# Kernel tuning notes

Measured on AMD Instinct MI355X. Metric: run time of the kernel, lower is better.

The kernel has to match this reference:

```python
import jax, jax.numpy as jnp
import numpy as np

B = 2048; E = 6; H = 4; D = 128; DH = D // H
LTXT = 24; CS = 20; JD = 7; SD = 16; LD = 32; K = 2
NLB = 4; NLD = 3; VOCAB = 512; DFF = 4 * D


def _ln(x, s, b, eps=1e-5):
    m = x.mean(-1, keepdims=True)
    v = ((x - m) ** 2).mean(-1, keepdims=True)
    return (x - m) * jax.lax.rsqrt(v + eps) * s + b


def _mha(xq, xkv, Wqkv, bqkv, Wo, bo, key_pad=None):
    # torch nn.MultiheadAttention, batch_first, eval (no dropout)
    Wq, Wk, Wv = jnp.split(Wqkv, 3, axis=-1)
    bq, bk, bv = jnp.split(bqkv, 3)
    Bc, Lq, _ = xq.shape
    Lk = xkv.shape[1]
    q = (xq @ Wq + bq).reshape(Bc, Lq, H, DH)
    k = (xkv @ Wk + bk).reshape(Bc, Lk, H, DH)
    v = (xkv @ Wv + bv).reshape(Bc, Lk, H, DH)
    s = jnp.einsum('bqhd,bkhd->bhqk', q, k) * (1.0 / DH ** 0.5)
    if key_pad is not None:
        s = jnp.where(key_pad[:, None, None, :], -1e9, s)
    a = jax.nn.softmax(s, axis=-1)
    o = jnp.einsum('bhqk,bkhd->bqhd', a, v).reshape(Bc, Lq, D)
    return o @ Wo + bo


def _sinusoidal_pe(L, d):
    pos = jnp.arange(L, dtype=jnp.float32)[:, None]
    div = jnp.exp(jnp.arange(0, d, 2, dtype=jnp.float32) * (-np.log(10000.0) / d))
    pe = jnp.zeros((L, d), jnp.float32)
    pe = pe.at[:, 0::2].set(jnp.sin(pos * div))
    return pe.at[:, 1::2].set(jnp.cos(pos * div))


def _forward(ids, state, tok_emb, pos_emb, bert_Wqkv, bert_bqkv, bert_Wo, bert_bo, bert_W1, bert_b1, bert_W2, bert_b2, bert_ln_s, bert_ln_b, bert_lnf_s, bert_lnf_b, se_W1, se_b1, se_W2, se_b2, se_ln_s, se_ln_b, r_W1, r_b1, r_W2, r_b2, r_ln_s, r_ln_b, gate_W, gate_b, exp_sp_W, exp_sp_b, exp_zp_W, exp_zp_b, exp_attn_Wqkv, exp_attn_bqkv, exp_attn_Wo, exp_attn_bo, exp_ln_s, exp_ln_b, exp_ff_W1, exp_ff_b1, exp_ff_W2, exp_ff_b2, exp_head_W, exp_head_b):
    Bc = ids.shape[0]
    gelu = lambda t: jax.nn.gelu(t, approximate=False)
    # ---- MiniBERT (post-LN encoder) ----
    pad = ids == 0  # PAD token
    x = tok_emb[ids] + pos_emb[None]  # [B,24,128]
    for l in range(NLB):
        a = _mha(x, x, bert_Wqkv[l], bert_bqkv[l], bert_Wo[l], bert_bo[l], pad)
        x = _ln(x + a, bert_ln_s[l, 0], bert_ln_b[l, 0])
        h = gelu(x @ bert_W1[l] + bert_b1[l]) @ bert_W2[l] + bert_b2[l]
        x = _ln(x + h, bert_ln_s[l, 1], bert_ln_b[l, 1])
    intent = _ln(x, bert_lnf_s, bert_lnf_b)[:, 0]  # CLS embedding [B,128]
    # ---- StateEncoder (MLP + LN) ----
    semb = _ln(gelu(state @ se_W1 + se_b1) @ se_W2 + se_b2, se_ln_s, se_ln_b)
    # ---- FusionRouter: top-k gating ----
    fused = _ln(gelu(jnp.concatenate([intent, semb], -1) @ r_W1 + r_b1) @ r_W2 + r_b2, r_ln_s, r_ln_b)
    logits = fused @ gate_W + gate_b  # [B,6]
    all_probs = jax.nn.softmax(logits, axis=-1)
    tv, ti = jax.lax.top_k(logits, K)
    weights = jax.nn.softmax(tv, axis=-1)  # [B,2]
    # ---- ACTExperts, inference path (z = 0) ----
    qpe = _sinusoidal_pe(CS, D)
    z = jnp.zeros((Bc, LD), state.dtype)

    def one_expert(sp_W, sp_b, zp_W, zp_b, aW, ab, oW, ob, lns, lnb, fW1, fb1, fW2, fb2, hW, hb):
        mem = jnp.stack([state @ sp_W + sp_b, z @ zp_W + zp_b], axis=1)  # [B,2,128]
        xq = jnp.broadcast_to(qpe[None], (Bc, CS, D))
        for l in range(NLD):  # norm_first decoder layers, relu FFN
            xn = _ln(xq, lns[l, 0], lnb[l, 0])
            xq = xq + _mha(xn, xn, aW[l, 0], ab[l, 0], oW[l, 0], ob[l, 0])
            xn = _ln(xq, lns[l, 1], lnb[l, 1])
            xq = xq + _mha(xn, mem, aW[l, 1], ab[l, 1], oW[l, 1], ob[l, 1])
            xn = _ln(xq, lns[l, 2], lnb[l, 2])
            xq = xq + jax.nn.relu(xn @ fW1[l] + fb1[l]) @ fW2[l] + fb2[l]
        return xq @ hW + hb  # [B,20,7]

    outs = jax.vmap(one_expert)(exp_sp_W, exp_sp_b, exp_zp_W, exp_zp_b, exp_attn_Wqkv, exp_attn_bqkv, exp_attn_Wo, exp_attn_bo, exp_ln_s, exp_ln_b, exp_ff_W1, exp_ff_b1, exp_ff_W2, exp_ff_b2, exp_head_W, exp_head_b)  # [E,B,20,7]
    # scatter top-k weights to a dense [B,E] gate and combine expert outputs
    w_full = jnp.zeros((Bc, E), logits.dtype).at[jnp.arange(Bc)[:, None], ti].add(weights)
    return jnp.einsum('be,ebtj->btj', w_full, outs)


def setup_inputs() -> dict:
    key = jax.random.key(0)
    it = iter(jax.random.split(key, 64))
    w = lambda *shape: jax.random.normal(next(it), shape, jnp.float32) * 0.05
    inp = {}
    inp['ids'] = jax.random.randint(next(it), (B, LTXT), 0, VOCAB, dtype=jnp.int32)
    inp['state'] = jax.random.normal(next(it), (B, SD), jnp.float32)
    inp['tok_emb'] = w(VOCAB, D).at[0].set(0.0)  # padding_idx=0
    inp['pos_emb'] = w(LTXT, D)
    inp['bert_Wqkv'] = w(NLB, D, 3 * D); inp['bert_bqkv'] = jnp.zeros((NLB, 3 * D))
    inp['bert_Wo'] = w(NLB, D, D); inp['bert_bo'] = jnp.zeros((NLB, D))
    inp['bert_W1'] = w(NLB, D, DFF); inp['bert_b1'] = jnp.zeros((NLB, DFF))
    inp['bert_W2'] = w(NLB, DFF, D); inp['bert_b2'] = jnp.zeros((NLB, D))
    inp['bert_ln_s'] = jnp.ones((NLB, 2, D)); inp['bert_ln_b'] = jnp.zeros((NLB, 2, D))
    inp['bert_lnf_s'] = jnp.ones((D,)); inp['bert_lnf_b'] = jnp.zeros((D,))
    inp['se_W1'] = w(SD, D); inp['se_b1'] = jnp.zeros((D,))
    inp['se_W2'] = w(D, D); inp['se_b2'] = jnp.zeros((D,))
    inp['se_ln_s'] = jnp.ones((D,)); inp['se_ln_b'] = jnp.zeros((D,))
    inp['r_W1'] = w(2 * D, D); inp['r_b1'] = jnp.zeros((D,))
    inp['r_W2'] = w(D, D); inp['r_b2'] = jnp.zeros((D,))
    inp['r_ln_s'] = jnp.ones((D,)); inp['r_ln_b'] = jnp.zeros((D,))
    inp['gate_W'] = w(D, E) * 10.0  # non-degenerate routing (source inits zeros)
    inp['gate_b'] = jnp.zeros((E,))
    inp['exp_sp_W'] = w(E, SD, D); inp['exp_sp_b'] = jnp.zeros((E, D))
    inp['exp_zp_W'] = w(E, LD, D); inp['exp_zp_b'] = jnp.zeros((E, D))
    inp['exp_attn_Wqkv'] = w(E, NLD, 2, D, 3 * D); inp['exp_attn_bqkv'] = jnp.zeros((E, NLD, 2, 3 * D))
    inp['exp_attn_Wo'] = w(E, NLD, 2, D, D); inp['exp_attn_bo'] = jnp.zeros((E, NLD, 2, D))
    inp['exp_ln_s'] = jnp.ones((E, NLD, 3, D)); inp['exp_ln_b'] = jnp.zeros((E, NLD, 3, D))
    inp['exp_ff_W1'] = w(E, NLD, D, DFF); inp['exp_ff_b1'] = jnp.zeros((E, NLD, DFF))
    inp['exp_ff_W2'] = w(E, NLD, DFF, D); inp['exp_ff_b2'] = jnp.zeros((E, NLD, D))
    inp['exp_head_W'] = w(E, D, JD); inp['exp_head_b'] = jnp.zeros((E, JD))
    return inp


def reference(ids, state, tok_emb, pos_emb, bert_Wqkv, bert_bqkv, bert_Wo, bert_bo, bert_W1, bert_b1, bert_W2, bert_b2, bert_ln_s, bert_ln_b, bert_lnf_s, bert_lnf_b, se_W1, se_b1, se_W2, se_b2, se_ln_s, se_ln_b, r_W1, r_b1, r_W2, r_b2, r_ln_s, r_ln_b, gate_W, gate_b, exp_sp_W, exp_sp_b, exp_zp_W, exp_zp_b, exp_attn_Wqkv, exp_attn_bqkv, exp_attn_Wo, exp_attn_bo, exp_ln_s, exp_ln_b, exp_ff_W1, exp_ff_b1, exp_ff_W2, exp_ff_b2, exp_head_W, exp_head_b):
    return _forward(ids, state, tok_emb, pos_emb, bert_Wqkv, bert_bqkv, bert_Wo, bert_bo, bert_W1, bert_b1, bert_W2, bert_b2, bert_ln_s, bert_ln_b, bert_lnf_s, bert_lnf_b, se_W1, se_b1, se_W2, se_b2, se_ln_s, se_ln_b, r_W1, r_b1, r_W2, r_b2, r_ln_s, r_ln_b, gate_W, gate_b, exp_sp_W, exp_sp_b, exp_zp_W, exp_zp_b, exp_attn_Wqkv, exp_attn_bqkv, exp_attn_Wo, exp_attn_bo, exp_ln_s, exp_ln_b, exp_ff_W1, exp_ff_b1, exp_ff_W2, exp_ff_b2, exp_head_W, exp_head_b)
```

## Files before the change

kernel.cpp:

```cpp
#include <hip/hip_runtime.h>
#include <math.h>

#define DEVI __device__ __forceinline__

namespace {

constexpr int Bn   = 2048;
constexpr int En   = 6;
constexpr int Hn   = 4;
constexpr int Dn   = 128;
constexpr int DHn  = 32;
constexpr int LTn  = 24;
constexpr int CSn  = 20;
constexpr int JDn  = 7;
constexpr int SDn  = 16;
constexpr int NLBn = 4;
constexpr int NLDn = 3;
constexpr int DFFn = 512;
constexpr float INV_SQRT_DH = 0.17677669529663687f;

constexpr int PAIRS  = 4096;
constexpr int MPMAX  = PAIRS * 20 + En * 128;
constexpr int NBGMAX = PAIRS * 20 / 128 + En;
constexpr int GEXP_OFF = 64;
constexpr int GMT_OFF  = 64 + NBGMAX;

constexpr int ROWSB = Bn * LTn;

constexpr int HSTR = 36;

typedef float f32x4v __attribute__((ext_vector_type(4)));
typedef short short8 __attribute__((ext_vector_type(8)));

DEVI float geluf(float x) { return 0.5f * x * (1.0f + erff(x * 0.70710678118654752f)); }

DEVI short f2bf(float f) {
  unsigned u = __float_as_uint(f);
  return (short)((u + 0x7FFFu + ((u >> 16) & 1u)) >> 16);
}
DEVI float bf2f(short s) { return __uint_as_float(((unsigned)(unsigned short)s) << 16); }
DEVI void split2(float v, short& h, short& l) {
  h = f2bf(v);
  l = f2bf(v - bf2f(h));
}

DEVI size_t apos(int row, int col, int KT) {
  return (((size_t)(row >> 4) * KT + (col >> 5)) * 64 + ((col >> 3) & 3) * 16 + (row & 15)) * 8
         + (col & 7);
}

__global__ void pack_kernel(const float* __restrict__ W, short* __restrict__ out,
                            const int K, const int N, const int total)
{
  const int p = (int)blockIdx.x * 256 + (int)threadIdx.x;
  if (p >= total) return;
  const int perMat = (K * N) >> 3;
  const int m = p / perMat, r = p - m * perMat;
  const int t = r >> 6, lane = r & 63;
  const int KT = K >> 5;
  const int nt = t / KT, kt = t - nt * KT;
  const int row0 = kt * 32 + (lane >> 4) * 8;
  const int col  = nt * 16 + (lane & 15);
  const float* src = W + (size_t)m * K * N;
  short8 v;
#pragma unroll
  for (int j = 0; j < 8; ++j) v[j] = f2bf(src[(size_t)(row0 + j) * N + col]);
  *reinterpret_cast<short8*>(out + (size_t)p * 8) = v;
}

__global__ void pack2_kernel(const float* __restrict__ W, short* __restrict__ out,
                             const int K, const int N, const int total)
{
  const int p = (int)blockIdx.x * 256 + (int)threadIdx.x;
  if (p >= total) return;
  const int perMat = (K * N) >> 3;
  const int m = p / perMat, r = p - m * perMat;
  const int t = r >> 6, lane = r & 63;
  const int KT = K >> 5;
  const int nt = t / KT, kt = t - nt * KT;
  const int row0 = kt * 32 + (lane >> 4) * 8;
  const int col  = nt * 16 + (lane & 15);
  const float* src = W + (size_t)m * K * N;
  short8 vh, vl;
#pragma unroll
  for (int j = 0; j < 8; ++j) {
    short hh, ll;
    split2(src[(size_t)(row0 + j) * N + col], hh, ll);
    vh[j] = hh; vl[j] = ll;
  }
  const size_t T  = (size_t)(perMat >> 6);
  const size_t tg = (size_t)m * T + t;
  *reinterpret_cast<short8*>(out + tg * 1024 + lane * 8)       = vh;
  *reinterpret_cast<short8*>(out + tg * 1024 + 512 + lane * 8) = vl;
}


__global__ __launch_bounds__(256) void bembed_kernel(
    const int* __restrict__ ids, const float* __restrict__ tok,
    const float* __restrict__ pos, float* __restrict__ X,
    short* __restrict__ Ah, short* __restrict__ Al)
{
  const int mt = (int)blockIdx.x;
  const int t = (int)threadIdx.x;
// ... 158 lines not shown
#pragma unroll
    for (int i = 0; i < 2; ++i) {
      f32x4v c = {0.f, 0.f, 0.f, 0.f};
#pragma unroll
      for (int kt = 0; kt < 4; ++kt) {
        c = __builtin_amdgcn_mfma_f32_16x16x32_bf16(ah[kt], bh[i][kt], c, 0, 0, 0);
        c = __builtin_amdgcn_mfma_f32_16x16x32_bf16(al[kt], bh[i][kt], c, 0, 0, 0);
        c = __builtin_amdgcn_mfma_f32_16x16x32_bf16(ah[kt], bl[i][kt], c, 0, 0, 0);
      }
      const int col = (wv * 2 + i) * 16 + r0;
      const float bb = bo[col];
#pragma unroll
      for (int q = 0; q < 4; ++q) {
        const int row = mtg * 16 + g * 4 + q;
        v[i][q] = c[q] + bb + X[(size_t)row * 128 + col];
      }
    }
    float s1[4], s2[4];
#pragma unroll
    for (int q = 0; q < 4; ++q) {
      s1[q] = v[0][q] + v[1][q];
      s2[q] = v[0][q] * v[0][q] + v[1][q] * v[1][q];
    }
#pragma unroll
    for (int o = 1; o < 16; o <<= 1)
#pragma unroll
      for (int q = 0; q < 4; ++q) { s1[q] += __shfl_xor(s1[q], o); s2[q] += __shfl_xor(s2[q], o); }
    if (r0 == 0)
#pragma unroll
      for (int q = 0; q < 4; ++q) { red[g * 4 + q][wv][0] = s1[q]; red[g * 4 + q][wv][1] = s2[q]; }
    __syncthreads();
#pragma unroll
    for (int q = 0; q < 4; ++q) {
      const int r = g * 4 + q;
      const float t1 = red[r][0][0] + red[r][1][0] + red[r][2][0] + red[r][3][0];
      const float t2 = red[r][0][1] + red[r][1][1] + red[r][2][1] + red[r][3][1];
      const float m  = t1 * (1.f / 128.f);
      const float rs = rsqrtf(t2 * (1.f / 128.f) - m * m + 1e-5f);
      const int row = mtg * 16 + r;
#pragma unroll
      for (int i = 0; i < 2; ++i) {
        const int col = (wv * 2 + i) * 16 + r0;
        const float o = (v[i][q] - m) * rs * gs[col] + gb[col];
        X[(size_t)row * 128 + col] = o;
        short hh, ll; split2(o, hh, ll);
        const size_t pk = apos(row, col, 4);
        OAh[pk] = hh; OAl[pk] = ll;
      }
    }
    __syncthreads();
  }
}

__global__ __launch_bounds__(256) void bw1_kernel(
    const short* __restrict__ Ah, const short* __restrict__ Al,
    const short* __restrict__ Bp, const float* __restrict__ bias,
    short* __restrict__ Hh, short* __restrict__ Hl)
{
  const int mt0 = (int)blockIdx.x * 4;
  const int nc  = (int)blockIdx.y;
  const int lane = (int)threadIdx.x & 63, wv = (int)threadIdx.x >> 6;
  const int r0 = lane & 15, g = lane >> 4;
  short8 bh[2][4], bl[2][4];
#pragma unroll
  for (int i = 0; i < 2; ++i)
#pragma unroll
    for (int kt = 0; kt < 4; ++kt) {
      const short* tb = Bp + (((size_t)(nc * 8 + wv * 2 + i) * 4 + kt) << 10);
      bh[i][kt] = *reinterpret_cast<const short8*>(tb + lane * 8);
      bl[i][kt] = *reinterpret_cast<const short8*>(tb + 512 + lane * 8);
    }
#pragma unroll 2
  for (int mt = 0; mt < 4; ++mt) {
    const int mtg = mt0 + mt;
    short8 ah[4], al[4];
#pragma unroll
    for (int kt = 0; kt < 4; ++kt) {
      ah[kt] = *reinterpret_cast<const short8*>(Ah + (((size_t)mtg * 4 + kt) * 64 + lane) * 8);
      al[kt] = *reinterpret_cast<const short8*>(Al + (((size_t)mtg * 4 + kt) * 64 + lane) * 8);
    }
#pragma unroll
    for (int i = 0; i < 2; ++i) {
      f32x4v c = {0.f, 0.f, 0.f, 0.f};
#pragma unroll
      for (int kt = 0; kt < 4; ++kt) {
        c = __builtin_amdgcn_mfma_f32_16x16x32_bf16(ah[kt], bh[i][kt], c, 0, 0, 0);
        c = __builtin_amdgcn_mfma_f32_16x16x32_bf16(al[kt], bh[i][kt], c, 0, 0, 0);
        c = __builtin_amdgcn_mfma_f32_16x16x32_bf16(ah[kt], bl[i][kt], c, 0, 0, 0);
      }
      const int col = nc * 128 + (wv * 2 + i) * 16 + r0;
      const float bb = bias[col];
#pragma unroll
      for (int q = 0; q < 4; ++q) {
        const int row = mtg * 16 + g * 4 + q;
        short hh, ll; split2(geluf(c[q] + bb), hh, ll);
        const size_t pk = apos(row, col, 16);
        Hh[pk] = hh; Hl[pk] = ll;
      }
    }
  }
}

__global__ __launch_bounds__(512) void bw2_kernel(
    const short* __restrict__ Hh, const short* __restrict__ Hl,
    const short* __restrict__ Bp, const float* __restrict__ bias,
    const float* __restrict__ gs, const float* __restrict__ gb,
    float* __restrict__ X, short* __restrict__ OAh, short* __restrict__ OAl)
{
  __shared__ float red[16][8][2];
  const int mt0 = (int)blockIdx.x * 4;
  const int lane = (int)threadIdx.x & 63, wv = (int)threadIdx.x >> 6;
  const int r0 = lane & 15, g = lane >> 4;
  f32x4v c[4];
#pragma unroll
  for (int mt = 0; mt < 4; ++mt) c[mt] = (f32x4v){0.f, 0.f, 0.f, 0.f};
#pragma unroll
  for (int half = 0; half < 2; ++half) {
    short8 bh[8], bl[8];
#pragma unroll
    for (int kk = 0; kk < 8; ++kk) {
      const short* tb = Bp + (((size_t)(wv * 16 + half * 8 + kk)) << 10);
      bh[kk] = *reinterpret_cast<const short8*>(tb + lane * 8);
      bl[kk] = *reinterpret_cast<const short8*>(tb + 512 + lane * 8);
    }
#pragma unroll
    for (int mt = 0; mt < 4; ++mt) {
      const int mtg = mt0 + mt;
#pragma unroll
      for (int kk = 0; kk < 8; ++kk) {
        const short8 ah = *reinterpret_cast<const short8*>(
            Hh + (((size_t)mtg * 16 + half * 8 + kk) * 64 + lane) * 8);
        const short8 al = *reinterpret_cast<const short8*>(
            Hl + (((size_t)mtg * 16 + half * 8 + kk) * 64 + lane) * 8);
        c[mt] = __builtin_amdgcn_mfma_f32_16x16x32_bf16(ah, bh[kk], c[mt], 0, 0, 0);
        c[mt] = __builtin_amdgcn_mfma_f32_16x16x32_bf16(al, bh[kk], c[mt], 0, 0, 0);
        c[mt] = __builtin_amdgcn_mfma_f32_16x16x32_bf16(ah, bl[kk], c[mt], 0, 0, 0);
      }
    }
  }
  const int col = wv * 16 + r0;
  const float bb = bias[col];
  for (int mt = 0; mt < 4; ++mt) {
    const int mtg = mt0 + mt;
    float v[4], s1[4], s2[4];
#pragma unroll
    for (int q = 0; q < 4; ++q) {
      const int row = mtg * 16 + g * 4 + q;
      v[q] = c[mt][q] + bb + X[(size_t)row * 128 + col];
      s1[q] = v[q]; s2[q] = v[q] * v[q];
    }
#pragma unroll
    for (int o = 1; o < 16; o <<= 1)
#pragma unroll
      for (int q = 0; q < 4; ++q) { s1[q] += __shfl_xor(s1[q], o); s2[q] += __shfl_xor(s2[q], o); }
    if (r0 == 0)
#pragma unroll
      for (int q = 0; q < 4; ++q) { red[g * 4 + q][wv][0] = s1[q]; red[g * 4 + q][wv][1] = s2[q]; }
    __syncthreads();
#pragma unroll
    for (int q = 0; q < 4; ++q) {
      const int r = g * 4 + q;
      float t1 = 0.f, t2 = 0.f;
#pragma unroll
      for (int w = 0; w < 8; ++w) { t1 += red[r][w][0]; t2 += red[r][w][1]; }
      const float m  = t1 * (1.f / 128.f);
      const float rs = rsqrtf(t2 * (1.f / 128.f) - m * m + 1e-5f);
      const int row = mtg * 16 + r;
      const float o = (v[q] - m) * rs * gs[col] + gb[col];
      X[(size_t)row * 128 + col] = o;
      short hh, ll; split2(o, hh, ll);
      const size_t pk = apos(row, col, 4);
      OAh[pk] = hh; OAl[pk] = ll;
    }
    __syncthreads();
  }
}

__global__ __launch_bounds__(256) void bintent_kernel(
    const float* __restrict__ X, const float* __restrict__ lnf_s,
    const float* __restrict__ lnf_b, float* __restrict__ intent)
{
  const int w = (int)threadIdx.x >> 6, lane = (int)threadIdx.x & 63;
  const int b = (int)blockIdx.x * 4 + w;
  const float* xr = X + (size_t)b * LTn * 128;
  const float a0 = xr[lane], a1 = xr[lane + 64];
  float s1 = a0 + a1, s2 = a0 * a0 + a1 * a1;
#pragma unroll
  for (int o = 32; o > 0; o >>= 1) { s1 += __shfl_xor(s1, o); s2 += __shfl_xor(s2, o); }
  const float m  = s1 * (1.f / 128.f);
  const float rs = rsqrtf(s2 * (1.f / 128.f) - m * m + 1e-5f);
  intent[b * 128 + lane]      = (a0 - m) * rs * lnf_s[lane]      + lnf_b[lane];
  intent[b * 128 + lane + 64] = (a1 - m) * rs * lnf_s[lane + 64] + lnf_b[lane + 64];
}

struct RouterP {
  const float* state; const float* intent;
  const float* se_W1; const float* se_b1; const float* se_W2; const float* se_b2;
  const float* se_ln_s; const float* se_ln_b;
  const float* r_W1; const float* r_b1; const float* r_W2; const float* r_b2;
  const float* r_ln_s; const float* r_ln_b;
  const float* gate_W; const float* gate_b;
// ... 207 lines not shown
  for (int k = 0; k < SDn; ++k) C[((size_t)li * SDn + k) * 256 + c2] = acc[k];
  k0c[li * 256 + c2] = bb[c2] + a0;
  k1c[li * 256 + c2] = bb[c2] + a1;
}

template<int NTW, int EPI, bool HASB>
__global__ __launch_bounds__(256) void gemm_k128(
    const short* __restrict__ A, const short* __restrict__ Bb, const int strideB,
    const float* __restrict__ biasb, const int strideBias, const int ntOff,
    short* __restrict__ OutBf, const int obstr, short* __restrict__ OutP,
    const float* __restrict__ lnsA, const float* __restrict__ lnbA, const int subOff,
    float* __restrict__ X, const int* __restrict__ sch)
{
  __shared__ float red[16][4][2];
  const int k = (int)blockIdx.x;
  if (k >= sch[0]) return;
  const int ex  = sch[GEXP_OFF + k];
  const int mt0 = sch[GMT_OFF + k] + (int)blockIdx.y * 4;
  const short* Bp = Bb + (size_t)ex * strideB;
  const float* bias = biasb + (size_t)ex * strideBias;
  const float* gs = (EPI == 4) ? lnsA + ex * (NLDn * 3 * 128) + subOff : nullptr;
  const float* gb = (EPI == 4) ? lnbA + ex * (NLDn * 3 * 128) + subOff : nullptr;
  const int lane = (int)threadIdx.x & 63, wv = (int)threadIdx.x >> 6;
  const int r0 = lane & 15, g = lane >> 4;
  short8 bf[NTW][4];
#pragma unroll
  for (int i = 0; i < NTW; ++i)
#pragma unroll
    for (int kt = 0; kt < 4; ++kt)
      bf[i][kt] = *reinterpret_cast<const short8*>(
          Bp + (((size_t)(ntOff + wv * NTW + i) * 4 + kt) * 64 + lane) * 8);
  for (int mt = 0; mt < 4; ++mt) {
    short8 a[4];
#pragma unroll
    for (int kt = 0; kt < 4; ++kt)
      a[kt] = *reinterpret_cast<const short8*>(
          A + (((size_t)(mt0 + mt) * 4 + kt) * 64 + lane) * 8);
    float v[NTW][4];
#pragma unroll
    for (int i = 0; i < NTW; ++i) {
      f32x4v c = {0.f, 0.f, 0.f, 0.f};
#pragma unroll
      for (int kt = 0; kt < 4; ++kt)
        c = __builtin_amdgcn_mfma_f32_16x16x32_bf16(a[kt], bf[i][kt], c, 0, 0, 0);
      const int colL = (wv * NTW + i) * 16 + r0;
      const float bb = HASB ? bias[colL] : 0.f;
      const int rowB = (mt0 + mt) * 16 + g * 4;
#pragma unroll
      for (int q = 0; q < 4; ++q) {
        const int row = rowB + q;
        const float val = c[q] + bb;
        if (EPI == 0) {
          OutBf[(size_t)row * obstr + colL] = f2bf(val);
        } else if (EPI == 3) {
          const float rv = fmaxf(val, 0.f);
          const int j = colL >> 3, kt2 = j >> 2, g2 = j & 3;
          const int lp = g2 * 16 + (row & 15);
          OutP[(((size_t)(row >> 4) * 16 + (ntOff >> 1) + kt2) * 64 + lp) * 8 + (colL & 7)]
              = f2bf(rv);
        } else {
          v[i][q] = val + X[(size_t)row * 128 + colL];
        }
      }
    }
    if (EPI == 4) {
      float s1[4], s2[4];
#pragma unroll
      for (int q = 0; q < 4; ++q) {
        s1[q] = v[0][q] + v[1][q];
        s2[q] = v[0][q] * v[0][q] + v[1][q] * v[1][q];
      }
#pragma unroll
      for (int o = 1; o < 16; o <<= 1)
#pragma unroll
        for (int q = 0; q < 4; ++q) { s1[q] += __shfl_xor(s1[q], o); s2[q] += __shfl_xor(s2[q], o); }
      if (r0 == 0)
#pragma unroll
        for (int q = 0; q < 4; ++q) { red[g * 4 + q][wv][0] = s1[q]; red[g * 4 + q][wv][1] = s2[q]; }
      __syncthreads();
#pragma unroll
      for (int q = 0; q < 4; ++q) {
        const int r = g * 4 + q;
        const float t1 = red[r][0][0] + red[r][1][0] + red[r][2][0] + red[r][3][0];
        const float t2 = red[r][0][1] + red[r][1][1] + red[r][2][1] + red[r][3][1];
        const float m  = t1 * (1.f / 128.f);
        const float rs = rsqrtf(t2 * (1.f / 128.f) - m * m + 1e-5f);
        const int row = (mt0 + mt) * 16 + r;
#pragma unroll
        for (int i = 0; i < 2; ++i) {
          const int col = (wv * 2 + i) * 16 + r0;
          const float o = (v[i][q] - m) * rs * gs[col] + gb[col];
          X[(size_t)row * 128 + col] = v[i][q];
          OutP[apos(row, col, 4)] = f2bf(o);
        }
      }
      __syncthreads();
    }
  }
}

template<bool DOLN>
__global__ __launch_bounds__(256) void gemm_k256f(
    const short* __restrict__ A, const short* __restrict__ Bb, const int strideB,
    const float* __restrict__ biasb, const int strideBias,
    float* __restrict__ X, short* __restrict__ OutP,
    const float* __restrict__ lnsA, const float* __restrict__ lnbA, const int subOff,
    const int* __restrict__ sch)
{
  __shared__ float red[16][4][2];
  const int k = (int)blockIdx.x;
  if (k >= sch[0]) return;
  const int ex  = sch[GEXP_OFF + k];
  const int mt0 = sch[GMT_OFF + k] + (int)blockIdx.y * 4;
  const short* Bp = Bb + (size_t)ex * strideB;
  const float* bias = biasb + (size_t)ex * strideBias;
  const float* gs = DOLN ? lnsA + ex * (NLDn * 3 * 128) + subOff : nullptr;
  const float* gb = DOLN ? lnbA + ex * (NLDn * 3 * 128) + subOff : nullptr;
  const int lane = (int)threadIdx.x & 63, wv = (int)threadIdx.x >> 6;
  const int r0 = lane & 15, g = lane >> 4;
  f32x4v c[4][2];
#pragma unroll
  for (int mtl = 0; mtl < 4; ++mtl)
#pragma unroll
    for (int i = 0; i < 2; ++i) c[mtl][i] = (f32x4v){0.f, 0.f, 0.f, 0.f};
#pragma unroll
  for (int half = 0; half < 2; ++half) {
    short8 bf[2][8];
#pragma unroll
    for (int i = 0; i < 2; ++i)
#pragma unroll
      for (int kk = 0; kk < 8; ++kk)
        bf[i][kk] = *reinterpret_cast<const short8*>(
            Bp + (((size_t)(wv * 2 + i) * 16 + half * 8 + kk) * 64 + lane) * 8);
#pragma unroll
    for (int mtl = 0; mtl < 4; ++mtl) {
      const int mtg = mt0 + mtl;
      short8 a[8];
#pragma unroll
      for (int kk = 0; kk < 8; ++kk)
        a[kk] = *reinterpret_cast<const short8*>(
            A + (((size_t)mtg * 16 + half * 8 + kk) * 64 + lane) * 8);
#pragma unroll
      for (int i = 0; i < 2; ++i)
#pragma unroll
        for (int kk = 0; kk < 8; ++kk)
          c[mtl][i] = __builtin_amdgcn_mfma_f32_16x16x32_bf16(a[kk], bf[i][kk], c[mtl][i], 0, 0, 0);
    }
  }
#pragma unroll
  for (int mtl = 0; mtl < 4; ++mtl) {
    const int mtg = mt0 + mtl;
    float v[2][4];
#pragma unroll
    for (int i = 0; i < 2; ++i) {
      const int colL = (wv * 2 + i) * 16 + r0;
      const float bb = bias[colL];
#pragma unroll
      for (int q = 0; q < 4; ++q) {
        const int row = mtg * 16 + g * 4 + q;
        v[i][q] = c[mtl][i][q] + bb + X[(size_t)row * 128 + colL];
      }
    }
    if (DOLN) {
      float s1[4], s2[4];
#pragma unroll
      for (int q = 0; q < 4; ++q) {
        s1[q] = v[0][q] + v[1][q];
        s2[q] = v[0][q] * v[0][q] + v[1][q] * v[1][q];
      }
#pragma unroll
      for (int o = 1; o < 16; o <<= 1)
#pragma unroll
        for (int q = 0; q < 4; ++q) { s1[q] += __shfl_xor(s1[q], o); s2[q] += __shfl_xor(s2[q], o); }
      if (r0 == 0)
#pragma unroll
        for (int q = 0; q < 4; ++q) { red[g * 4 + q][wv][0] = s1[q]; red[g * 4 + q][wv][1] = s2[q]; }
      __syncthreads();
#pragma unroll
      for (int q = 0; q < 4; ++q) {
        const int r = g * 4 + q;
        const float t1 = red[r][0][0] + red[r][1][0] + red[r][2][0] + red[r][3][0];
        const float t2 = red[r][0][1] + red[r][1][1] + red[r][2][1] + red[r][3][1];
        const float m  = t1 * (1.f / 128.f);
        const float rs = rsqrtf(t2 * (1.f / 128.f) - m * m + 1e-5f);
        const int row = mtg * 16 + r;
#pragma unroll
        for (int i = 0; i < 2; ++i) {
          const int col = (wv * 2 + i) * 16 + r0;
          const float o = (v[i][q] - m) * rs * gs[col] + gb[col];
          X[(size_t)row * 128 + col] = v[i][q];
          OutP[apos(row, col, 4)] = f2bf(o);
        }
      }
      __syncthreads();
    } else {
#pragma unroll
      for (int i = 0; i < 2; ++i) {
        const int colL = (wv * 2 + i) * 16 + r0;
#pragma unroll
        for (int q = 0; q < 4; ++q) {
          const int row = mtg * 16 + g * 4 + q;
          X[(size_t)row * 128 + colL] = v[i][q];
        }
      }
    }
  }
}

__global__ __launch_bounds__(64) void sattn_kernel(
    const short* __restrict__ QKVb, const int* __restrict__ prow,
    short* __restrict__ ANP)
{
  __shared__ float qs[CSn * HSTR], ks[CSn * HSTR], vs[CSn * HSTR];
  __shared__ float att[CSn * CSn];
  __shared__ float inv[CSn];
  const int i = (int)blockIdx.x, h = (int)blockIdx.y;
  const int tid = (int)threadIdx.x;
  const int row0 = prow[i];
  for (int u = tid; u < CSn * 12; u += 64) {
    const int il = u / 12, r = u % 12, which = r >> 2, d8 = r & 3;
    const short8 s = *reinterpret_cast<const short8*>(
        QKVb + (size_t)(row0 + il) * 384 + which * 128 + h * 32 + d8 * 8);
    float* dst = (which == 0 ? qs : which == 1 ? ks : vs) + il * HSTR + d8 * 8;
#pragma unroll
    for (int u8 = 0; u8 < 8; ++u8) dst[u8] = bf2f(s[u8]);
  }
  __syncthreads();
  for (int e = tid; e < CSn * CSn; e += 64) {
    const int ii = e / CSn, j = e % CSn;
    const float* qp = qs + ii * HSTR;
    const float* kp = ks + j * HSTR;
    float acc = 0.f;
#pragma unroll
    for (int d = 0; d < DHn; d += 4) {
      const float4 qa = *reinterpret_cast<const float4*>(qp + d);
      const float4 kb = *reinterpret_cast<const float4*>(kp + d);
      acc += qa.x * kb.x + qa.y * kb.y + qa.z * kb.z + qa.w * kb.w;
    }
    att[e] = acc * INV_SQRT_DH;
  }
  __syncthreads();
  if (tid < 2 * CSn) {
    const int r = tid >> 1, h0 = (tid & 1) * 10;
    float* row = att + r * CSn + h0;
    float m = row[0];
#pragma unroll
    for (int j = 1; j < 10; ++j) m = fmaxf(m, row[j]);
    m = fmaxf(m, __shfl_xor(m, 1));
    float s = 0.f;
#pragma unroll
    for (int j = 0; j < 10; ++j) { const float ex = expf(row[j] - m); row[j] = ex; s += ex; }
    s += __shfl_xor(s, 1);
    if ((tid & 1) == 0) inv[r] = 1.f / s;
  }
  __syncthreads();
  for (int e = tid; e < CSn * 32; e += 64) {
// ... 118 lines not shown
    const int t = e >> 7, d = e & 127;
    const float j  = (float)(d & ~1);
    const float dv = expf(j * (-logf(10000.f) / 128.f));
    const float a  = (float)t * dv;
    qpe[e] = (d & 1) ? cosf(a) : sinf(a);
  }
}

}

extern "C" void kernel_launch(void* const* d_in, const int* in_sizes, int n_in,
                              void* d_out, int out_size, void* d_ws, size_t ws_size,
                              hipStream_t stream)
{
  (void)in_sizes; (void)n_in; (void)out_size;

  const int*   ids     = (const int*)  d_in[0];
  const float* state   = (const float*)d_in[1];
  const float* tok_emb = (const float*)d_in[2];
  const float* pos_emb = (const float*)d_in[3];

  char* cur = (char*)d_ws;
  auto alloc = [&cur](size_t bytes) -> char* {
    char* p = cur; cur += (bytes + 255) & ~(size_t)255; return p;
  };
  float* qpe    = (float*)alloc(4096 * 4);
  float* intent = (float*)alloc((size_t)Bn * Dn * 4);
  int*   ridx   = (int*)  alloc(PAIRS * 4);
  float* rwgt   = (float*)alloc(PAIRS * 4);
  short* pQ     = (short*)alloc((size_t)36 * 49152 * 2);
  short* pO     = (short*)alloc((size_t)36 * 16384 * 2);
  short* pF1    = (short*)alloc((size_t)18 * 65536 * 2);
  short* pF2    = (short*)alloc((size_t)18 * 65536 * 2);
  short* pbQ    = (short*)alloc((size_t)4 * 98304 * 2);
  short* pbO    = (short*)alloc((size_t)4 * 32768 * 2);
  short* pbW1   = (short*)alloc((size_t)4 * 131072 * 2);
  short* pbW2   = (short*)alloc((size_t)4 * 131072 * 2);
  int*   sch    = (int*)  alloc(2048 * 4);
  int*   plist  = (int*)  alloc(PAIRS * 4);
  int*   prow   = (int*)  alloc(PAIRS * 4);
  int*   pexp   = (int*)  alloc(PAIRS * 4);
  int*   ppos   = (int*)  alloc(PAIRS * 4);
  float* Cmat   = (float*)alloc((size_t)18 * SDn * 256 * 4);
  float* k0c    = (float*)alloc((size_t)18 * 256 * 4);
  float* k1c    = (float*)alloc((size_t)18 * 256 * 4);
  constexpr size_t ARENA_BYTES = 192806912;
  char* arena = alloc(ARENA_BYTES);
  if ((size_t)(cur - (char*)d_ws) > ws_size) return;

  float* Xb  = (float*)(arena);
  short* Ah  = (short*)(arena + 25165824);
  short* Al  = (short*)(arena + 37748736);
  float* SBb = (float*)(arena + 50331648);
  short* Hh  = (short*)(arena + 50331648);
  short* Hl  = (short*)(arena + 100663296);
  float* X2   = (float*)(arena);
  short* ANP  = (short*)(arena + 42336256);
  short* SBh  = (short*)(arena + 63504384);
  float* Rbuf = (float*)(arena + 190513152);

  qpe_kernel<<<dim3(10), dim3(256), 0, stream>>>(qpe);

  {
    const int tq = 36 * 6144;
    pack_kernel<<<dim3((tq + 255) / 256), dim3(256), 0, stream>>>(
        (const float*)d_in[34], pQ, 128, 384, tq);
    const int to = 36 * 2048;
    pack_kernel<<<dim3((to + 255) / 256), dim3(256), 0, stream>>>(
        (const float*)d_in[36], pO, 128, 128, to);
    const int t1c = 18 * 8192;
    pack_kernel<<<dim3((t1c + 255) / 256), dim3(256), 0, stream>>>(
        (const float*)d_in[40], pF1, 128, 512, t1c);
    const int t2c = 18 * 8192;
    pack_kernel<<<dim3((t2c + 255) / 256), dim3(256), 0, stream>>>(
        (const float*)d_in[42], pF2, 512, 128, t2c);
    const int bq = 4 * 6144;
    pack2_kernel<<<dim3((bq + 255) / 256), dim3(256), 0, stream>>>(
        (const float*)d_in[4], pbQ, 128, 384, bq);
    const int bo = 4 * 2048;
    pack2_kernel<<<dim3((bo + 255) / 256), dim3(256), 0, stream>>>(
        (const float*)d_in[6], pbO, 128, 128, bo);
    const int bw1 = 4 * 8192;
    pack2_kernel<<<dim3((bw1 + 255) / 256), dim3(256), 0, stream>>>(
        (const float*)d_in[8], pbW1, 128, 512, bw1);
    const int bw2 = 4 * 8192;
    pack2_kernel<<<dim3((bw2 + 255) / 256), dim3(256), 0, stream>>>(
        (const float*)d_in[10], pbW2, 512, 128, bw2);
    compose_kernel<<<dim3(En * NLDn), dim3(256), 0, stream>>>(
        (const float*)d_in[30], (const float*)d_in[31], (const float*)d_in[33],
        (const float*)d_in[34], (const float*)d_in[35], Cmat, k0c, k1c);
  }

  {
    const float* bq  = (const float*)d_in[5];
    const float* bo  = (const float*)d_in[7];
    const float* b1  = (const float*)d_in[9];
    const float* b2  = (const float*)d_in[11];
    const float* lns = (const float*)d_in[12];
    const float* lnb = (const float*)d_in[13];

    bembed_kernel<<<dim3(ROWSB / 16), dim3(256), 0, stream>>>(
        ids, tok_emb, pos_emb, Xb, Ah, Al);
    for (int l = 0; l < NLBn; ++l) {
      bqkv_kernel<<<dim3(ROWSB / 64, 3), dim3(256), 0, stream>>>(
          Ah, Al, pbQ + (size_t)l * 98304, bq + l * 384, SBb);
      battn_kernel<<<dim3(Bn, Hn), dim3(64), 0, stream>>>(SBb, ids, Ah, Al);
      bo_ln_kernel<<<dim3(ROWSB / 64), dim3(256), 0, stream>>>(
          Ah, Al, pbO + (size_t)l * 32768, bo + l * 128,
          lns + l * 256, lnb + l * 256, Xb, Ah, Al);
      bw1_kernel<<<dim3(ROWSB / 64, 4), dim3(256), 0, stream>>>(
          Ah, Al, pbW1 + (size_t)l * 131072, b1 + l * 512, Hh, Hl);
      bw2_kernel<<<dim3(ROWSB / 64), dim3(512), 0, stream>>>(
          Hh, Hl, pbW2 + (size_t)l * 131072, b2 + l * 128,
          lns + l * 256 + 128, lnb + l * 256 + 128, Xb, Ah, Al);
    }
    bintent_kernel<<<dim3(Bn / 4), dim3(256), 0, stream>>>(
        Xb, (const float*)d_in[14], (const float*)d_in[15], intent);
  }

  {
    RouterP rp;
    rp.state = state; rp.intent = intent;
    rp.se_W1 = (const float*)d_in[16]; rp.se_b1 = (const float*)d_in[17];
    rp.se_W2 = (const float*)d_in[18]; rp.se_b2 = (const float*)d_in[19];
    rp.se_ln_s = (const float*)d_in[20]; rp.se_ln_b = (const float*)d_in[21];
    rp.r_W1 = (const float*)d_in[22]; rp.r_b1 = (const float*)d_in[23];
    rp.r_W2 = (const float*)d_in[24]; rp.r_b2 = (const float*)d_in[25];
    rp.r_ln_s = (const float*)d_in[26]; rp.r_ln_b = (const float*)d_in[27];
    rp.gate_W = (const float*)d_in[28]; rp.gate_b = (const float*)d_in[29];
    rp.ridx = ridx; rp.rwgt = rwgt;
    router_kernel<<<dim3(Bn), dim3(128), 0, stream>>>(rp);
  }

  const float* ab   = (const float*)d_in[35];
  const float* abo  = (const float*)d_in[37];
  const float* lnsA = (const float*)d_in[38];
  const float* lnbA = (const float*)d_in[39];
  const float* fb1A = (const float*)d_in[41];
  const float* fb2A = (const float*)d_in[43];
  const float* hW   = (const float*)d_in[44];
  const float* hB   = (const float*)d_in[45];

  {
    sched_kernel<<<dim3(1), dim3(256), 0, stream>>>(ridx, sch, plist, prow, pexp, ppos);
    xinit_kernel<<<dim3(MPMAX * 32 / 256), dim3(256), 0, stream>>>(qpe, sch, X2);
    ln_pack_kernel<<<dim3(MPMAX / 16), dim3(256), 0, stream>>>(
        X2, ANP, lnsA, lnbA, 0, sch);
    short* HP = SBh;
    for (int l = 0; l < NLDn; ++l) {
      gemm_k128<6, 0, true><<<dim3(NBGMAX, 2), dim3(256), 0, stream>>>(
          ANP, pQ + (l * 2 + 0) * 49152, 294912,
          ab + (l * 2 + 0) * 384, 2304, 0,
          SBh, 384, nullptr, nullptr, nullptr, 0, nullptr, sch);
      sattn_kernel<<<dim3(PAIRS, Hn), dim3(64), 0, stream>>>(SBh, prow, ANP);
      gemm_k128<2, 4, true><<<dim3(NBGMAX, 2), dim3(256), 0, stream>>>(
          ANP, pO + (l * 2 + 0) * 16384, 98304,
          abo + (l * 2 + 0) * 128, 768, 0,
          nullptr, 0, ANP, lnsA, lnbA, (l * 3 + 1) * 128, X2, sch);
      gemm_k128<2, 0, true><<<dim3(NBGMAX, 2), dim3(256), 0, stream>>>(
          ANP, pQ + (l * 2 + 1) * 49152, 294912,
          ab + (l * 2 + 1) * 384, 2304, 0,
          SBh, 128, nullptr, nullptr, nullptr, 0, nullptr, sch);
      cattn_kernel<<<dim3(PAIRS), dim3(256), 0, stream>>>(
          SBh, state, Cmat, k0c, k1c, l, plist, prow, pexp, ANP);
      gemm_k128<2, 4, true><<<dim3(NBGMAX, 2), dim3(256), 0, stream>>>(
          ANP, pO + (l * 2 + 1) * 16384, 98304,
          abo + (l * 2 + 1) * 128, 768, 0,
          nullptr, 0, ANP, lnsA, lnbA, (l * 3 + 2) * 128, X2, sch);
      gemm_k128<4, 3, true><<<dim3(NBGMAX, 2), dim3(256), 0, stream>>>(
          ANP, pF1 + l * 65536, 196608,
          fb1A + l * 512 + 0 * 256, 1536, 0,
          nullptr, 0, HP, nullptr, nullptr, 0, nullptr, sch);
      gemm_k128<4, 3, true><<<dim3(NBGMAX, 2), dim3(256), 0, stream>>>(
          ANP, pF1 + l * 65536, 196608,
          fb1A + l * 512 + 1 * 256, 1536, 16,
          nullptr, 0, HP, nullptr, nullptr, 0, nullptr, sch);
      if (l < NLDn - 1) {
        gemm_k256f<true><<<dim3(NBGMAX, 2), dim3(256), 0, stream>>>(
            HP, pF2 + l * 65536, 196608, fb2A + l * 128, 384,
            X2, ANP, lnsA, lnbA, ((l + 1) * 3 + 0) * 128, sch);
      } else {
        gemm_k256f<false><<<dim3(NBGMAX, 2), dim3(256), 0, stream>>>(
            HP, pF2 + l * 65536, 196608, fb2A + l * 128, 384,
            X2, nullptr, nullptr, nullptr, 0, sch);
      }
    }
    head_kernel<<<dim3(PAIRS), dim3(256), 0, stream>>>(
        X2, plist, prow, pexp, rwgt, hW, hB, Rbuf);
    combine_kernel<<<dim3((Bn * 140 + 255) / 256), dim3(256), 0, stream>>>(
        Rbuf, ppos, (float*)d_out);
  }
}
```

Before: 1.625 ms.

## Fuse FFN up and down projections into single kernels with LDS-resident hidden

Merges the BERT FFN's two kernels (W1+GELU, then W2+residual+LN) into one 512-thread kernel that keeps the 32-row GELU hidden tile, split into high and low bf16 parts, in shared memory. It does the same for the expert FFN, replacing two ReLU GEMM launches and the K=256 down-projection with one kernel that holds a 64-row hidden tile in LDS. This removes the global write and read of the 512-wide hidden activations and several launches. In exchange it uses large LDS allocations that may limit occupancy, reloads W1/W2 weights per block, and processes fewer rows per block in the BERT path.

```diff
diff --git a/kernel.cpp b/kernel.cpp
--- a/kernel.cpp
+++ b/kernel.cpp
@@ -49,6 +49,11 @@
          + (col & 7);
 }
 
+DEVI size_t hpos(int rl, int col) {
+  return (((size_t)((rl >> 4) * 16 + (col >> 5)) * 64) + ((col >> 3) & 3) * 16 + (rl & 15)) * 8
+         + (col & 7);
+}
+
 __global__ void pack_kernel(const float* __restrict__ W, short* __restrict__ out,
                             const int K, const int N, const int total)
 {
@@ -313,101 +318,87 @@
   }
 }
 
-__global__ __launch_bounds__(256) void bw1_kernel(
+__global__ __launch_bounds__(512) void bffn_kernel(
     const short* __restrict__ Ah, const short* __restrict__ Al,
-    const short* __restrict__ Bp, const float* __restrict__ bias,
-    short* __restrict__ Hh, short* __restrict__ Hl)
-{
-  const int mt0 = (int)blockIdx.x * 4;
-  const int nc  = (int)blockIdx.y;
+    const short* __restrict__ W1p, const short* __restrict__ W2p,
+    const float* __restrict__ b1, const float* __restrict__ b2,
+    const float* __restrict__ gs, const float* __restrict__ gb,
+    float* __restrict__ X, short* __restrict__ OAh, short* __restrict__ OAl)
+{
+  __shared__ short HhL[2 * 16 * 64 * 8];
+  __shared__ short HlL[2 * 16 * 64 * 8];
+  __shared__ float red[16][8][2];
+  const int mtg0 = (int)blockIdx.x * 2;
   const int lane = (int)threadIdx.x & 63, wv = (int)threadIdx.x >> 6;
   const int r0 = lane & 15, g = lane >> 4;
-  short8 bh[2][4], bl[2][4];
-#pragma unroll
-  for (int i = 0; i < 2; ++i)
+  short8 ah[2][4], al[2][4];
+#pragma unroll
+  for (int mtl = 0; mtl < 2; ++mtl)
 #pragma unroll
     for (int kt = 0; kt < 4; ++kt) {
-      const short* tb = Bp + (((size_t)(nc * 8 + wv * 2 + i) * 4 + kt) << 10);
-      bh[i][kt] = *reinterpret_cast<const short8*>(tb + lane * 8);
-      bl[i][kt] = *reinterpret_cast<const short8*>(tb + 512 + lane * 8);
-    }
-#pragma unroll 2
-  for (int mt = 0; mt < 4; ++mt) {
-    const int mtg = mt0 + mt;
-    short8 ah[4], al[4];
+      ah[mtl][kt] = *reinterpret_cast<const short8*>(
+          Ah + (((size_t)(mtg0 + mtl) * 4 + kt) * 64 + lane) * 8);
+      al[mtl][kt] = *reinterpret_cast<const short8*>(
+          Al + (((size_t)(mtg0 + mtl) * 4 + kt) * 64 + lane) * 8);
+    }
+#pragma unroll
+  for (int i = 0; i < 4; ++i) {
+    const int nt = wv * 4 + i;
+    short8 bh[4], bl[4];
 #pragma unroll
     for (int kt = 0; kt < 4; ++kt) {
-      ah[kt] = *reinterpret_cast<const short8*>(Ah + (((size_t)mtg * 4 + kt) * 64 + lane) * 8);
-      al[kt] = *reinterpret_cast<const short8*>(Al + (((size_t)mtg * 4 + kt) * 64 + lane) * 8);
-    }
-#pragma unroll
-    for (int i = 0; i < 2; ++i) {
+      const short* tb = W1p + (((size_t)(nt * 4 + kt)) << 10);
+      bh[kt] = *reinterpret_cast<const short8*>(tb + lane * 8);
+      bl[kt] = *reinterpret_cast<const short8*>(tb + 512 + lane * 8);
+    }
+    const int col = nt * 16 + r0;
+    const float bb = b1[col];
+#pragma unroll
+    for (int mtl = 0; mtl < 2; ++mtl) {
       f32x4v c = {0.f, 0.f, 0.f, 0.f};
 #pragma unroll
       for (int kt = 0; kt < 4; ++kt) {
-        c = __builtin_amdgcn_mfma_f32_16x16x32_bf16(ah[kt], bh[i][kt], c, 0, 0, 0);
-        c = __builtin_amdgcn_mfma_f32_16x16x32_bf16(al[kt], bh[i][kt], c, 0, 0, 0);
-        c = __builtin_amdgcn_mfma_f32_16x16x32_bf16(ah[kt], bl[i][kt], c, 0, 0, 0);
-      }
-      const int col = nc * 128 + (wv * 2 + i) * 16 + r0;
-      const float bb = bias[col];
+        c = __builtin_amdgcn_mfma_f32_16x16x32_bf16(ah[mtl][kt], bh[kt], c, 0, 0, 0);
+        c = __builtin_amdgcn_mfma_f32_16x16x32_bf16(al[mtl][kt], bh[kt], c, 0, 0, 0);
+        c = __builtin_amdgcn_mfma_f32_16x16x32_bf16(ah[mtl][kt], bl[kt], c, 0, 0, 0);
+      }
 #pragma unroll
       for (int q = 0; q < 4; ++q) {
-        const int row = mtg * 16 + g * 4 + q;
+        const int rl = mtl * 16 + g * 4 + q;
         short hh, ll; split2(geluf(c[q] + bb), hh, ll);
-        const size_t pk = apos(row, col, 16);
-        Hh[pk] = hh; Hl[pk] = ll;
-      }
-    }
-  }
-}
-
-__global__ __launch_bounds__(512) void bw2_kernel(
-    const short* __restrict__ Hh, const short* __restrict__ Hl,
-    const short* __restrict__ Bp, const float* __restrict__ bias,
-    const float* __restrict__ gs, const float* __restrict__ gb,
-    float* __restrict__ X, short* __restrict__ OAh, short* __restrict__ OAl)
-{
-  __shared__ float red[16][8][2];
-  const int mt0 = (int)blockIdx.x * 4;
-  const int lane = (int)threadIdx.x & 63, wv = (int)threadIdx.x >> 6;
-  const int r0 = lane & 15, g = lane >> 4;
-  f32x4v c[4];
-#pragma unroll
-  for (int mt = 0; mt < 4; ++mt) c[mt] = (f32x4v){0.f, 0.f, 0.f, 0.f};
-#pragma unroll
-  for (int half = 0; half < 2; ++half) {
-    short8 bh[8], bl[8];
-#pragma unroll
-    for (int kk = 0; kk < 8; ++kk) {
-      const short* tb = Bp + (((size_t)(wv * 16 + half * 8 + kk)) << 10);
-      bh[kk] = *reinterpret_cast<const short8*>(tb + lane * 8);
-      bl[kk] = *reinterpret_cast<const short8*>(tb + 512 + lane * 8);
-    }
-#pragma unroll
-    for (int mt = 0; mt < 4; ++mt) {
-      const int mtg = mt0 + mt;
-#pragma unroll
-      for (int kk = 0; kk < 8; ++kk) {
-        const short8 ah = *reinterpret_cast<const short8*>(
-            Hh + (((size_t)mtg * 16 + half * 8 + kk) * 64 + lane) * 8);
-        const short8 al = *reinterpret_cast<const short8*>(
-            Hl + (((size_t)mtg * 16 + half * 8 + kk) * 64 + lane) * 8);
-        c[mt] = __builtin_amdgcn_mfma_f32_16x16x32_bf16(ah, bh[kk], c[mt], 0, 0, 0);
-        c[mt] = __builtin_amdgcn_mfma_f32_16x16x32_bf16(al, bh[kk], c[mt], 0, 0, 0);
-        c[mt] = __builtin_amdgcn_mfma_f32_16x16x32_bf16(ah, bl[kk], c[mt], 0, 0, 0);
-      }
-    }
-  }
+        const size_t hp = hpos(rl, col);
+        HhL[hp] = hh; HlL[hp] = ll;
+      }
+    }
+  }
+  __syncthreads();
   const int col = wv * 16 + r0;
-  const float bb = bias[col];
-  for (int mt = 0; mt < 4; ++mt) {
-    const int mtg = mt0 + mt;
+  f32x4v c2[2];
+#pragma unroll
+  for (int mtl = 0; mtl < 2; ++mtl) c2[mtl] = (f32x4v){0.f, 0.f, 0.f, 0.f};
+#pragma unroll
+  for (int kk = 0; kk < 16; ++kk) {
+    const short* tb = W2p + (((size_t)(wv * 16 + kk)) << 10);
+    const short8 b2h = *reinterpret_cast<const short8*>(tb + lane * 8);
+    const short8 b2l = *reinterpret_cast<const short8*>(tb + 512 + lane * 8);
+#pragma unroll
+    for (int mtl = 0; mtl < 2; ++mtl) {
+      const size_t ap = (((size_t)(mtl * 16 + kk) * 64 + lane)) * 8;
+      const short8 a2h = *reinterpret_cast<const short8*>(HhL + ap);
+      const short8 a2l = *reinterpret_cast<const short8*>(HlL + ap);
+      c2[mtl] = __builtin_amdgcn_mfma_f32_16x16x32_bf16(a2h, b2h, c2[mtl], 0, 0, 0);
+      c2[mtl] = __builtin_amdgcn_mfma_f32_16x16x32_bf16(a2l, b2h, c2[mtl], 0, 0, 0);
+      c2[mtl] = __builtin_amdgcn_mfma_f32_16x16x32_bf16(a2h, b2l, c2[mtl], 0, 0, 0);
+    }
+  }
+  const float bb2 = b2[col];
+  for (int mtl = 0; mtl < 2; ++mtl) {
+    const int mtg = mtg0 + mtl;
     float v[4], s1[4], s2[4];
 #pragma unroll
     for (int q = 0; q < 4; ++q) {
       const int row = mtg * 16 + g * 4 + q;
-      v[q] = c[mt][q] + bb + X[(size_t)row * 128 + col];
+      v[q] = c2[mtl][q] + bb2 + X[(size_t)row * 128 + col];
       s1[q] = v[q]; s2[q] = v[q] * v[q];
     }
 #pragma unroll
@@ -721,12 +712,6 @@
         const float val = c[q] + bb;
         if (EPI == 0) {
           OutBf[(size_t)row * obstr + colL] = f2bf(val);
-        } else if (EPI == 3) {
-          const float rv = fmaxf(val, 0.f);
-          const int j = colL >> 3, kt2 = j >> 2, g2 = j & 3;
-          const int lp = g2 * 16 + (row & 15);
-          OutP[(((size_t)(row >> 4) * 16 + (ntOff >> 1) + kt2) * 64 + lp) * 8 + (colL & 7)]
-              = f2bf(rv);
         } else {
           v[i][q] = val + X[(size_t)row * 128 + colL];
         }
@@ -769,74 +754,88 @@
 }
 
 template<bool DOLN>
-__global__ __launch_bounds__(256) void gemm_k256f(
-    const short* __restrict__ A, const short* __restrict__ Bb, const int strideB,
-    const float* __restrict__ biasb, const int strideBias,
+__global__ __launch_bounds__(512) void effn_kernel(
+    const short* __restrict__ A, const short* __restrict__ W1b, const int strideW1,
+    const float* __restrict__ b1b, const int strideB1,
+    const short* __restrict__ W2b, const int strideW2,
+    const float* __restrict__ b2b, const int strideB2,
     float* __restrict__ X, short* __restrict__ OutP,
     const float* __restrict__ lnsA, const float* __restrict__ lnbA, const int subOff,
     const int* __restrict__ sch)
 {
-  __shared__ float red[16][4][2];
+  __shared__ short HsL[4 * 16 * 64 * 8];
+  __shared__ float red[16][8][2];
   const int k = (int)blockIdx.x;
   if (k >= sch[0]) return;
   const int ex  = sch[GEXP_OFF + k];
   const int mt0 = sch[GMT_OFF + k] + (int)blockIdx.y * 4;
-  const short* Bp = Bb + (size_t)ex * strideB;
-  const float* bias = biasb + (size_t)ex * strideBias;
+  const short* W1p = W1b + (size_t)ex * strideW1;
+  const short* W2p = W2b + (size_t)ex * strideW2;
+  const float* b1 = b1b + (size_t)ex * strideB1;
+  const float* b2 = b2b + (size_t)ex * strideB2;
   const float* gs = DOLN ? lnsA + ex * (NLDn * 3 * 128) + subOff : nullptr;
   const float* gb = DOLN ? lnbA + ex * (NLDn * 3 * 128) + subOff : nullptr;
   const int lane = (int)threadIdx.x & 63, wv = (int)threadIdx.x >> 6;
   const int r0 = lane & 15, g = lane >> 4;
-  f32x4v c[4][2];
+  short8 a[4][4];
 #pragma unroll
   for (int mtl = 0; mtl < 4; ++mtl)
 #pragma unroll
-    for (int i = 0; i < 2; ++i) c[mtl][i] = (f32x4v){0.f, 0.f, 0.f, 0.f};
-#pragma unroll
-  for (int half = 0; half < 2; ++half) {
-    short8 bf[2][8];
-#pragma unroll
-    for (int i = 0; i < 2; ++i)
-#pragma unroll
-      for (int kk = 0; kk < 8; ++kk)
-        bf[i][kk] = *reinterpret_cast<const short8*>(
-            Bp + (((size_t)(wv * 2 + i) * 16 + half * 8 + kk) * 64 + lane) * 8);
+    for (int kt = 0; kt < 4; ++kt)
+      a[mtl][kt] = *reinterpret_cast<const short8*>(
+          A + (((size_t)(mt0 + mtl) * 4 + kt) * 64 + lane) * 8);
+#pragma unroll
+  for (int i = 0; i < 4; ++i) {
+    const int nt = wv * 4 + i;
+    short8 bw[4];
+#pragma unroll
+    for (int kt = 0; kt < 4; ++kt)
+      bw[kt] = *reinterpret_cast<const short8*>(
+          W1p + (((size_t)(nt * 4 + kt) * 64 + lane)) * 8);
+    const int col = nt * 16 + r0;
+    const float bb = b1[col];
 #pragma unroll
     for (int mtl = 0; mtl < 4; ++mtl) {
-      const int mtg = mt0 + mtl;
-      short8 a[8];
-#pragma unroll
-      for (int kk = 0; kk < 8; ++kk)
-        a[kk] = *reinterpret_cast<const short8*>(
-            A + (((size_t)mtg * 16 + half * 8 + kk) * 64 + lane) * 8);
-#pragma unroll
-      for (int i = 0; i < 2; ++i)
-#pragma unroll
-        for (int kk = 0; kk < 8; ++kk)
-          c[mtl][i] = __builtin_amdgcn_mfma_f32_16x16x32_bf16(a[kk], bf[i][kk], c[mtl][i], 0, 0, 0);
-    }
-  }
-#pragma unroll
+      f32x4v c = {0.f, 0.f, 0.f, 0.f};
+#pragma unroll
+      for (int kt = 0; kt < 4; ++kt)
+        c = __builtin_amdgcn_mfma_f32_16x16x32_bf16(a[mtl][kt], bw[kt], c, 0, 0, 0);
+#pragma unroll
+      for (int q = 0; q < 4; ++q) {
+        const int rl = mtl * 16 + g * 4 + q;
+        HsL[hpos(rl, col)] = f2bf(fmaxf(c[q] + bb, 0.f));
+      }
+    }
+  }
+  __syncthreads();
+  const int col = wv * 16 + r0;
+  f32x4v c2[4];
+#pragma unroll
+  for (int mtl = 0; mtl < 4; ++mtl) c2[mtl] = (f32x4v){0.f, 0.f, 0.f, 0.f};
+#pragma unroll
+  for (int kk = 0; kk < 16; ++kk) {
+    const short8 bw = *reinterpret_cast<const short8*>(
+        W2p + (((size_t)(wv * 16 + kk) * 64 + lane)) * 8);
+#pragma unroll
+    for (int mtl = 0; mtl < 4; ++mtl) {
+      const short8 aw = *reinterpret_cast<const short8*>(
+          HsL + (((size_t)(mtl * 16 + kk) * 64 + lane)) * 8);
+      c2[mtl] = __builtin_amdgcn_mfma_f32_16x16x32_bf16(aw, bw, c2[mtl], 0, 0, 0);
+    }
+  }
+  const float bb2 = b2[col];
   for (int mtl = 0; mtl < 4; ++mtl) {
     const int mtg = mt0 + mtl;
-    float v[2][4];
-#pragma unroll
-    for (int i = 0; i < 2; ++i) {
-      const int colL = (wv * 2 + i) * 16 + r0;
-      const float bb = bias[colL];
-#pragma unroll
-      for (int q = 0; q < 4; ++q) {
-        const int row = mtg * 16 + g * 4 + q;
-        v[i][q] = c[mtl][i][q] + bb + X[(size_t)row * 128 + colL];
-      }
+    float v[4];
+#pragma unroll
+    for (int q = 0; q < 4; ++q) {
+      const int row = mtg * 16 + g * 4 + q;
+      v[q] = c2[mtl][q] + bb2 + X[(size_t)row * 128 + col];
     }
     if (DOLN) {
       float s1[4], s2[4];
 #pragma unroll
-      for (int q = 0; q < 4; ++q) {
-        s1[q] = v[0][q] + v[1][q];
-        s2[q] = v[0][q] * v[0][q] + v[1][q] * v[1][q];
-      }
+      for (int q = 0; q < 4; ++q) { s1[q] = v[q]; s2[q] = v[q] * v[q]; }
 #pragma unroll
       for (int o = 1; o < 16; o <<= 1)
 #pragma unroll
@@ -848,29 +847,22 @@
 #pragma unroll
       for (int q = 0; q < 4; ++q) {
         const int r = g * 4 + q;
-        const float t1 = red[r][0][0] + red[r][1][0] + red[r][2][0] + red[r][3][0];
-        const float t2 = red[r][0][1] + red[r][1][1] + red[r][2][1] + red[r][3][1];
+        float t1 = 0.f, t2 = 0.f;
+#pragma unroll
+        for (int w = 0; w < 8; ++w) { t1 += red[r][w][0]; t2 += red[r][w][1]; }
         const float m  = t1 * (1.f / 128.f);
         const float rs = rsqrtf(t2 * (1.f / 128.f) - m * m + 1e-5f);
         const int row = mtg * 16 + r;
-#pragma unroll
-        for (int i = 0; i < 2; ++i) {
-          const int col = (wv * 2 + i) * 16 + r0;
-          const float o = (v[i][q] - m) * rs * gs[col] + gb[col];
-          X[(size_t)row * 128 + col] = v[i][q];
-          OutP[apos(row, col, 4)] = f2bf(o);
-        }
+        const float o = (v[q] - m) * rs * gs[col] + gb[col];
+        X[(size_t)row * 128 + col] = v[q];
+        OutP[apos(row, col, 4)] = f2bf(o);
       }
       __syncthreads();
     } else {
 #pragma unroll
-      for (int i = 0; i < 2; ++i) {
-        const int colL = (wv * 2 + i) * 16 + r0;
-#pragma unroll
-        for (int q = 0; q < 4; ++q) {
-          const int row = mtg * 16 + g * 4 + q;
-          X[(size_t)row * 128 + colL] = v[i][q];
-        }
+      for (int q = 0; q < 4; ++q) {
+        const int row = mtg * 16 + g * 4 + q;
+        X[(size_t)row * 128 + col] = v[q];
       }
     }
   }
@@ -1095,8 +1087,6 @@
   short* Ah  = (short*)(arena + 25165824);
   short* Al  = (short*)(arena + 37748736);
   float* SBb = (float*)(arena + 50331648);
-  short* Hh  = (short*)(arena + 50331648);
-  short* Hl  = (short*)(arena + 100663296);
   float* X2   = (float*)(arena);
   short* ANP  = (short*)(arena + 42336256);
   short* SBh  = (short*)(arena + 63504384);
@@ -1151,10 +1141,9 @@
       bo_ln_kernel<<<dim3(ROWSB / 64), dim3(256), 0, stream>>>(
           Ah, Al, pbO + (size_t)l * 32768, bo + l * 128,
           lns + l * 256, lnb + l * 256, Xb, Ah, Al);
-      bw1_kernel<<<dim3(ROWSB / 64, 4), dim3(256), 0, stream>>>(
-          Ah, Al, pbW1 + (size_t)l * 131072, b1 + l * 512, Hh, Hl);
-      bw2_kernel<<<dim3(ROWSB / 64), dim3(512), 0, stream>>>(
-          Hh, Hl, pbW2 + (size_t)l * 131072, b2 + l * 128,
+      bffn_kernel<<<dim3(ROWSB / 32), dim3(512), 0, stream>>>(
+          Ah, Al, pbW1 + (size_t)l * 131072, pbW2 + (size_t)l * 131072,
+          b1 + l * 512, b2 + l * 128,
           lns + l * 256 + 128, lnb + l * 256 + 128, Xb, Ah, Al);
     }
     bintent_kernel<<<dim3(Bn / 4), dim3(256), 0, stream>>>(
@@ -1189,7 +1178,6 @@
     xinit_kernel<<<dim3(MPMAX * 32 / 256), dim3(256), 0, stream>>>(qpe, sch, X2);
     ln_pack_kernel<<<dim3(MPMAX / 16), dim3(256), 0, stream>>>(
         X2, ANP, lnsA, lnbA, 0, sch);
-    short* HP = SBh;
     for (int l = 0; l < NLDn; ++l) {
       gemm_k128<6, 0, true><<<dim3(NBGMAX, 2), dim3(256), 0, stream>>>(
           ANP, pQ + (l * 2 + 0) * 49152, 294912,
@@ -1210,21 +1198,15 @@
           ANP, pO + (l * 2 + 1) * 16384, 98304,
           abo + (l * 2 + 1) * 128, 768, 0,
           nullptr, 0, ANP, lnsA, lnbA, (l * 3 + 2) * 128, X2, sch);
-      gemm_k128<4, 3, true><<<dim3(NBGMAX, 2), dim3(256), 0, stream>>>(
-          ANP, pF1 + l * 65536, 196608,
-          fb1A + l * 512 + 0 * 256, 1536, 0,
-          nullptr, 0, HP, nullptr, nullptr, 0, nullptr, sch);
-      gemm_k128<4, 3, true><<<dim3(NBGMAX, 2), dim3(256), 0, stream>>>(
-          ANP, pF1 + l * 65536, 196608,
-          fb1A + l * 512 + 1 * 256, 1536, 16,
-          nullptr, 0, HP, nullptr, nullptr, 0, nullptr, sch);
       if (l < NLDn - 1) {
-        gemm_k256f<true><<<dim3(NBGMAX, 2), dim3(256), 0, stream>>>(
-            HP, pF2 + l * 65536, 196608, fb2A + l * 128, 384,
+        effn_kernel<true><<<dim3(NBGMAX, 2), dim3(512), 0, stream>>>(
+            ANP, pF1 + l * 65536, 196608, fb1A + l * 512, 1536,
+            pF2 + l * 65536, 196608, fb2A + l * 128, 384,
             X2, ANP, lnsA, lnbA, ((l + 1) * 3 + 0) * 128, sch);
       } else {
-        gemm_k256f<false><<<dim3(NBGMAX, 2), dim3(256), 0, stream>>>(
-            HP, pF2 + l * 65536, 196608, fb2A + l * 128, 384,
+        effn_kernel<false><<<dim3(NBGMAX, 2), dim3(512), 0, stream>>>(
+            ANP, pF1 + l * 65536, 196608, fb1A + l * 512, 1536,
+            pF2 + l * 65536, 196608, fb2A + l * 128, 384,
             X2, nullptr, nullptr, nullptr, 0, sch);
       }
     }
```

Measured after the change: 1.410 ms, median of 4. 13.2% less time.
